# Kernel optimization log

Hardware: AMD Instinct MI355X
Metric: run time of the kernel (lower is better)

## Reference

```python
import jax, jax.numpy as jnp
import numpy as np

N_NODES = 50000
N_REL = 4
N_EDGE = 160000
H = 128
OUT = 100
L_HID = 2
N_QUERY = 8192


def setup_inputs() -> dict:
    key = jax.random.key(0)
    ks = jax.random.split(key, 10)
    s = 1.0 / np.sqrt(H)
    return {
        "feature": jax.random.normal(ks[0], (N_NODES, H), dtype=jnp.float32),
        "Wr_h": jax.random.normal(ks[1], (L_HID, N_REL, H, H), dtype=jnp.float32) * s,
        "Ws_h": jax.random.normal(ks[2], (L_HID, H, H), dtype=jnp.float32) * s,
        "Wr_o": jax.random.normal(ks[3], (N_REL, H, OUT), dtype=jnp.float32) * s,
        "Ws_o": jax.random.normal(ks[4], (H, OUT), dtype=jnp.float32) * s,
        "edge_src": jax.random.randint(ks[5], (N_REL, N_EDGE), 0, N_NODES, dtype=jnp.int64),
        "edge_dst": jax.random.randint(ks[6], (N_REL, N_EDGE), 0, N_NODES, dtype=jnp.int64),
        "head_idx": jax.random.randint(ks[7], (N_QUERY,), 0, N_NODES, dtype=jnp.int64),
        "tail_idx": jax.random.randint(ks[8], (N_QUERY,), 0, N_NODES, dtype=jnp.int64),
    }


def _rgcn_layer(h, edge_src, edge_dst, inv_deg, Wr, Ws, activate):
    # per-relation gather of source features: [R, E, H]
    msgs = h[edge_src]
    # per-relation scatter-add into destination nodes: [R, N, H]
    agg = jax.vmap(lambda m, d: jax.ops.segment_sum(m, d, num_segments=h.shape[0]))(msgs, edge_dst)
    agg = agg * inv_deg[..., None]  # mean (right) normalization per relation
    out = h @ Ws + jnp.einsum("rnh,rho->no", agg, Wr)
    return jax.nn.relu(out) if activate else out


def reference(feature, Wr_h, Ws_h, Wr_o, Ws_o, edge_src, edge_dst, head_idx, tail_idx):
    n = feature.shape[0]
    # per-relation in-degree, computed once (graph structure is fixed)
    deg = jax.vmap(lambda d: jax.ops.segment_sum(
        jnp.ones(d.shape, feature.dtype), d, num_segments=n))(edge_dst)  # [R, N]
    inv_deg = 1.0 / jnp.maximum(deg, 1.0)
    h = feature
    for l in range(Wr_h.shape[0]):
        h = _rgcn_layer(h, edge_src, edge_dst, inv_deg, Wr_h[l], Ws_h[l], activate=True)
    h = _rgcn_layer(h, edge_src, edge_dst, inv_deg, Wr_o, Ws_o, activate=False)
    heads = h[head_idx]  # [Q, OUT]
    tails = h[tail_idx]  # [Q, OUT]
    return (heads, tails)
```

## Files before the change

### kernel.cpp

```cpp
#include <hip/hip_runtime.h>
#include <hip/hip_bf16.h>

#define NN 50000
#define NR 4
#define NE 160000
#define HD 128
#define OD 100
#define NQ 8192
#define ELL_CAP 16
#define OVF_CAP 8192

#define NB_BUILD 2500
#define NB_CONV  6250
#define NB_PREPW 960

typedef __attribute__((ext_vector_type(8))) short bf16x8;
typedef __attribute__((ext_vector_type(4))) float f32x4;
typedef __attribute__((ext_vector_type(2))) float f32x2;
typedef __attribute__((ext_vector_type(4))) int int4v;

static __device__ __forceinline__ unsigned short f2bf(float f) {
    union { float f; unsigned int u; } v; v.f = f;
    unsigned int u = v.u;
    unsigned int r = u + 0x7FFFu + ((u >> 16) & 1u);
    return (unsigned short)(r >> 16);
}
static __device__ __forceinline__ float bflo(unsigned int v) {
    union { unsigned int u; float f; } x; x.u = v << 16; return x.f;
}
static __device__ __forceinline__ float bfhi(unsigned int v) {
    union { unsigned int u; float f; } x; x.u = v & 0xffff0000u; return x.f;
}


__global__ __launch_bounds__(256) void prep_merged_kernel(
        const int* __restrict__ edge_src, const int* __restrict__ edge_dst,
        int* __restrict__ deg, int* __restrict__ ell,
        int* __restrict__ ovf_cnt, int2* __restrict__ ovf,
        const float* __restrict__ feature, unsigned short* __restrict__ h,
        const float* __restrict__ Ws_h, const float* __restrict__ Wr_h,
        const float* __restrict__ Ws_o, const float* __restrict__ Wr_o,
        unsigned short* __restrict__ Wt) {
    const int b = blockIdx.x;
    if (b < NB_BUILD) {
        const int i = b * 256 + threadIdx.x;
        const int r = i / NE;
        const int key = (edge_dst[i] << 2) | r;
        const int src = edge_src[i];
        const int pos = atomicAdd(&deg[key], 1);
        if (pos < ELL_CAP) ell[key * ELL_CAP + pos] = src;
        else {
            const int op = atomicAdd(ovf_cnt, 1);
            if (op < OVF_CAP) ovf[op] = make_int2(key, src);
        }
    } else if (b < NB_BUILD + NB_CONV) {
        const int i = ((b - NB_BUILD) * 256 + threadIdx.x) * 4;
        h[i + 0] = f2bf(feature[i + 0]);
        h[i + 1] = f2bf(feature[i + 1]);
        h[i + 2] = f2bf(feature[i + 2]);
        h[i + 3] = f2bf(feature[i + 3]);
    } else {
        const int idx = (b - NB_BUILD - NB_CONV) * 256 + threadIdx.x;
        const int l = idx / (128 * 640);
        const int rem = idx % (128 * 640);
        const int c = rem / 640;
        const int k = rem % 640;
        float v = 0.0f;
        if (l < 2) {
            if (k < HD) v = Ws_h[(l * HD + k) * HD + c];
            else {
                int r = (k - HD) >> 7, kk = (k - HD) & 127;
                v = Wr_h[((l * NR + r) * HD + kk) * HD + c];
            }
        } else if (c < OD) {
            if (k < HD) v = Ws_o[k * OD + c];
            else {
                int r = (k - HD) >> 7, kk = (k - HD) & 127;
                v = Wr_o[(r * HD + kk) * OD + c];
            }
        }
        Wt[idx] = f2bf(v);
    }
}


template<int MODE>
__global__ __launch_bounds__(512, 8)
void fused_kernel(const unsigned short* __restrict__ h,
                  const unsigned short* __restrict__ Bt,
                  const int* __restrict__ deg,
                  const int* __restrict__ ell,
                  const int* __restrict__ ovf_cnt,
                  const int2* __restrict__ ovf,
                  void* __restrict__ outp, int M) {
    __shared__ __align__(16) char lds[40960];
    const int tid = threadIdx.x;
    const int m0 = blockIdx.x * 32;
    const int lane = tid & 63;
    const int w = tid >> 6;

    {
        const int row = tid >> 4, kb = (tid & 15) * 16;
        int gr = m0 + row; if (gr >= M) gr = M - 1;
        int4v v = *(const int4v*)((const char*)h + (size_t)gr * 256 + kb);
        *(int4v*)(lds + row * 256 + (kb ^ ((row & 7) << 4))) = v;
    }

    {
        const int g = lane >> 4, li = lane & 15;
        const char* hp = (const char*)h + li * 16;
        const int n0 = m0 + (w << 2);

#pragma unroll 1
        for (int i = 0; i < 4; ++i) {
            const int n = n0 + i;
            const int nc = (n < M) ? n : (M - 1);
            const int key = (nc << 2) | g;
            const int dg = (n < M) ? deg[key] : 0;
            const int e = (dg < ELL_CAP) ? dg : ELL_CAP;
            const int* eb = ell + ((size_t)key << 4);

            const int4v s03 = *(const int4v*)(eb);
            const int4v s47 = *(const int4v*)(eb + 4);

            int4v vj[8];
            const int4v z = {0, 0, 0, 0};
#pragma unroll
            for (int j = 0; j < 4; j++)
                vj[j] = (j < e) ? *(const int4v*)(hp + (size_t)s03[j] * 256) : z;
#pragma unroll
            for (int j = 0; j < 4; j++)
                vj[4 + j] = (4 + j < e) ? *(const int4v*)(hp + (size_t)s47[j] * 256) : z;
            __builtin_amdgcn_sched_barrier(0);

            f32x2 c0 = {0.f, 0.f}, c1 = {0.f, 0.f}, c2 = {0.f, 0.f}, c3 = {0.f, 0.f};
#pragma unroll
            for (int j = 0; j < 8; j++) {
                const unsigned int* vu = (const unsigned int*)&vj[j];
                c0 += (f32x2){bflo(vu[0]), bfhi(vu[0])};
                c1 += (f32x2){bflo(vu[1]), bfhi(vu[1])};
                c2 += (f32x2){bflo(vu[2]), bfhi(vu[2])};
                c3 += (f32x2){bflo(vu[3]), bfhi(vu[3])};
            }

            if (dg > 8) {
                const int4v s8  = *(const int4v*)(eb + 8);
                const int4v s12 = *(const int4v*)(eb + 12);
                int4v wj[8];
#pragma unroll
                for (int j = 0; j < 4; j++)
                    wj[j] = (8 + j < e) ? *(const int4v*)(hp + (size_t)s8[j] * 256) : z;
#pragma unroll
                for (int j = 0; j < 4; j++)
                    wj[4 + j] = (12 + j < e) ? *(const int4v*)(hp + (size_t)s12[j] * 256) : z;
#pragma unroll
                for (int j = 0; j < 8; j++) {
                    const unsigned int* vu = (const unsigned int*)&wj[j];
                    c0 += (f32x2){bflo(vu[0]), bfhi(vu[0])};
                    c1 += (f32x2){bflo(vu[1]), bfhi(vu[1])};
                    c2 += (f32x2){bflo(vu[2]), bfhi(vu[2])};
                    c3 += (f32x2){bflo(vu[3]), bfhi(vu[3])};
                }
            }

            if (dg > ELL_CAP) {
                int oc = ovf_cnt[0];
                if (oc > OVF_CAP) oc = OVF_CAP;
                for (int k = 0; k < oc; ++k) {
                    const int2 ov = ovf[k];
                    if (ov.x == key) {
                        const int4v v = *(const int4v*)(hp + (size_t)ov.y * 256);
                        const unsigned int* vu = (const unsigned int*)&v;
                        c0 += (f32x2){bflo(vu[0]), bfhi(vu[0])};
                        c1 += (f32x2){bflo(vu[1]), bfhi(vu[1])};
                        c2 += (f32x2){bflo(vu[2]), bfhi(vu[2])};
                        c3 += (f32x2){bflo(vu[3]), bfhi(vu[3])};
                    }
                }
            }

            const float inv = 1.0f / fmaxf((float)dg, 1.0f);
            unsigned int p0 = (unsigned int)f2bf(inv * c0[0]) | ((unsigned int)f2bf(inv * c0[1]) << 16);
            unsigned int p1 = (unsigned int)f2bf(inv * c1[0]) | ((unsigned int)f2bf(inv * c1[1]) << 16);
            unsigned int p2 = (unsigned int)f2bf(inv * c2[0]) | ((unsigned int)f2bf(inv * c2[1]) << 16);
            unsigned int p3 = (unsigned int)f2bf(inv * c3[0]) | ((unsigned int)f2bf(inv * c3[1]) << 16);
            const int row = (w << 2) + i;
            const int cb = g * 256 + li * 16;
            *(int4v*)(lds + 8192 + row * 1024 + (cb ^ ((row & 7) << 4))) =
                (int4v){(int)p0, (int)p1, (int)p2, (int)p3};
        }
    }

    const int lr = lane & 15;
    const int lg = lane >> 4;
    const char* bB = (const char*)Bt + (size_t)(w * 16 + lr) * 1280;
    bf16x8 bpre[4];
#pragma unroll
    for (int kb = 0; kb < 4; kb++)
        bpre[kb] = *(const bf16x8*)(bB + kb * 64 + lg * 16);

    __syncthreads();

    f32x4 acc[2];
    acc[0] = (f32x4){0.f, 0.f, 0.f, 0.f};
    acc[1] = (f32x4){0.f, 0.f, 0.f, 0.f};

    __builtin_amdgcn_s_setprio(1);
#pragma unroll
    for (int kb = 0; kb < 20; ++kb) {
        const int kByte = kb * 64 + lg * 16;
        bf16x8 bfr = (kb < 4) ? bpre[kb] : *(const bf16x8*)(bB + kByte);
#pragma unroll
        for (int mi = 0; mi < 2; mi++) {
            const int row = mi * 16 + lr;
            int off;
            if (kb < 4) off = row * 256 + (kByte ^ ((row & 7) << 4));
            else        off = 8192 + row * 1024 + ((kByte - 256) ^ ((row & 7) << 4));
            bf16x8 af = *(const bf16x8*)(lds + off);
            acc[mi] = __builtin_amdgcn_mfma_f32_16x16x32_bf16(af, bfr, acc[mi], 0, 0, 0);
        }
    }
    __builtin_amdgcn_s_setprio(0);

    __syncthreads();

    if (MODE == 0) {
#pragma unroll
        for (int mi = 0; mi < 2; mi++) {
            const int col = w * 16 + lr;
#pragma unroll
            for (int j = 0; j < 4; j++) {
                const int row = mi * 16 + lg * 4 + j;
                *(unsigned short*)(lds + row * 256 + ((col * 2) ^ ((row & 7) << 4))) =
                    f2bf(fmaxf(acc[mi][j], 0.f));
            }
        }
        __syncthreads();
        unsigned short* o = (unsigned short*)outp;
        const int row = tid >> 4, kb = (tid & 15) * 16;
        const int grow = m0 + row;
        if (grow < M)
            *(int4v*)((char*)o + (size_t)grow * 256 + kb) =
                *(const int4v*)(lds + row * 256 + (kb ^ ((row & 7) << 4)));
    } else {
#pragma unroll
        for (int mi = 0; mi < 2; mi++) {
            const int col = w * 16 + lr;
#pragma unroll
            for (int j = 0; j < 4; j++) {
                const int row = mi * 16 + lg * 4 + j;
                *(float*)(lds + row * 512 + ((col * 4) ^ ((row & 7) << 4))) = acc[mi][j];
            }
        }
        __syncthreads();
        float* o = (float*)outp;
#pragma unroll
        for (int i = 0; i < 2; i++) {
            const int c = tid + i * 512;
            const int row = c >> 5, o16 = (c & 31) * 16;
            const int grow = m0 + row;
            if (grow < M)
                *(int4v*)((char*)o + (size_t)grow * 512 + o16) =
                    *(const int4v*)(lds + row * 512 + (o16 ^ ((row & 7) << 4)));
        }
    }
}


__global__ __launch_bounds__(256) void gather_out_kernel(const float* __restrict__ hOut,
                                                         const int* __restrict__ head,
                                                         const int* __restrict__ tail,
                                                         float* __restrict__ out) {
    const int gid = blockIdx.x * 256 + threadIdx.x;
    const int q = gid >> 5, c = gid & 31;
    if (q >= 2 * NQ || c >= 25) return;
    const int node = (q < NQ) ? head[q] : tail[q - NQ];
    f32x4 v = *(const f32x4*)(hOut + (size_t)node * 128 + c * 4);
    *(f32x4*)(out + (size_t)q * OD + c * 4) = v;
}


extern "C" void kernel_launch(void* const* d_in, const int* in_sizes, int n_in,
                              void* d_out, int out_size, void* d_ws, size_t ws_size,
                              hipStream_t stream) {
    const float* feature = (const float*)d_in[0];
    const float* Wr_h    = (const float*)d_in[1];
    const float* Ws_h    = (const float*)d_in[2];
    const float* Wr_o    = (const float*)d_in[3];
    const float* Ws_o    = (const float*)d_in[4];
    const int* edge_src  = (const int*)d_in[5];
    const int* edge_dst  = (const int*)d_in[6];
    const int* head_idx  = (const int*)d_in[7];
    const int* tail_idx  = (const int*)d_in[8];
    float* out = (float*)d_out;

    char* ws = (char*)d_ws;
    size_t off = 0;
    auto alloc = [&](size_t bytes) -> void* {
        void* p = ws + off;
        off += (bytes + 255) & ~(size_t)255;
        return p;
    };
    unsigned short* hA   = (unsigned short*)alloc((size_t)NN * HD * 2);
    unsigned short* hB   = (unsigned short*)alloc((size_t)NN * HD * 2);
    float*          hOut = (float*)alloc((size_t)NN * 128 * 4);
    unsigned short* Wt   = (unsigned short*)alloc((size_t)3 * 128 * 640 * 2);
    int*            deg  = (int*)alloc((size_t)NR * NN * 4);
    int*            ovfc = (int*)alloc(256);
    int*            ell  = (int*)alloc((size_t)NR * NN * ELL_CAP * 4);
    int2*           ovf  = (int2*)alloc((size_t)OVF_CAP * 8);
    (void)ws_size;

    hipMemsetAsync(deg, 0, (size_t)NR * NN * 4 + 256, stream);
    prep_merged_kernel<<<NB_BUILD + NB_CONV + NB_PREPW, 256, 0, stream>>>(
        edge_src, edge_dst, deg, ell, ovfc, ovf,
        feature, hA, Ws_h, Wr_h, Ws_o, Wr_o, Wt);

    const int fblocks = (NN + 31) / 32;
    unsigned short* WtH0 = Wt;
    unsigned short* WtH1 = Wt + 128 * 640;
    unsigned short* WtO  = Wt + 2 * 128 * 640;

    fused_kernel<0><<<fblocks, 512, 0, stream>>>(hA, WtH0, deg, ell, ovfc, ovf, hB, NN);
    fused_kernel<0><<<fblocks, 512, 0, stream>>>(hB, WtH1, deg, ell, ovfc, ovf, hA, NN);
    fused_kernel<1><<<fblocks, 512, 0, stream>>>(hA, WtO,  deg, ell, ovfc, ovf, hOut, NN);

    gather_out_kernel<<<(2 * NQ * 32 + 255) / 256, 256, 0, stream>>>(hOut, head_idx, tail_idx, out);
}
```

Baseline: 220.6 us.

## Split ELL into lo/hi halves and double block threads to 1024

The ELL adjacency table is split into two arrays of 8 slots each, so the common low-degree path reads a compact 32-byte row and only touches the high half when degree exceeds 8. The fused aggregate+GEMM kernel moves to 1024 threads per block. Each wave now aggregates 2 nodes instead of 4, with both nodes' degree and index loads hoisted ahead of the loop, and computes one 16x16 MFMA tile instead of two. The sched_barrier is removed. The aim is more memory-level parallelism in the irregular gather and less serial work per wave. The cost is a tighter register budget per thread under launch_bounds(1024,2) and more waves competing for the same LDS tile.

```diff
diff --git a/kernel.cpp b/kernel.cpp
--- a/kernel.cpp
+++ b/kernel.cpp
@@ -35,7 +35,7 @@
 
 __global__ __launch_bounds__(256) void prep_merged_kernel(
         const int* __restrict__ edge_src, const int* __restrict__ edge_dst,
-        int* __restrict__ deg, int* __restrict__ ell,
+        int* __restrict__ deg, int* __restrict__ ell_lo, int* __restrict__ ell_hi,
         int* __restrict__ ovf_cnt, int2* __restrict__ ovf,
         const float* __restrict__ feature, unsigned short* __restrict__ h,
         const float* __restrict__ Ws_h, const float* __restrict__ Wr_h,
@@ -48,7 +48,8 @@
         const int key = (edge_dst[i] << 2) | r;
         const int src = edge_src[i];
         const int pos = atomicAdd(&deg[key], 1);
-        if (pos < ELL_CAP) ell[key * ELL_CAP + pos] = src;
+        if (pos < 8)             ell_lo[key * 8 + pos] = src;
+        else if (pos < ELL_CAP)  ell_hi[key * 8 + (pos - 8)] = src;
         else {
             const int op = atomicAdd(ovf_cnt, 1);
             if (op < OVF_CAP) ovf[op] = make_int2(key, src);
@@ -85,11 +86,12 @@
 
 
 template<int MODE>
-__global__ __launch_bounds__(512, 8)
+__global__ __launch_bounds__(1024, 2)
 void fused_kernel(const unsigned short* __restrict__ h,
                   const unsigned short* __restrict__ Bt,
                   const int* __restrict__ deg,
-                  const int* __restrict__ ell,
+                  const int* __restrict__ ell_lo,
+                  const int* __restrict__ ell_hi,
                   const int* __restrict__ ovf_cnt,
                   const int2* __restrict__ ovf,
                   void* __restrict__ outp, int M) {
@@ -99,7 +101,7 @@
     const int lane = tid & 63;
     const int w = tid >> 6;
 
-    {
+    if (tid < 512) {
         const int row = tid >> 4, kb = (tid & 15) * 16;
         int gr = m0 + row; if (gr >= M) gr = M - 1;
         int4v v = *(const int4v*)((const char*)h + (size_t)gr * 256 + kb);
@@ -109,29 +111,33 @@
     {
         const int g = lane >> 4, li = lane & 15;
         const char* hp = (const char*)h + li * 16;
-        const int n0 = m0 + (w << 2);
-
-#pragma unroll 1
-        for (int i = 0; i < 4; ++i) {
-            const int n = n0 + i;
-            const int nc = (n < M) ? n : (M - 1);
-            const int key = (nc << 2) | g;
-            const int dg = (n < M) ? deg[key] : 0;
-            const int e = (dg < ELL_CAP) ? dg : ELL_CAP;
-            const int* eb = ell + ((size_t)key << 4);
-
-            const int4v s03 = *(const int4v*)(eb);
-            const int4v s47 = *(const int4v*)(eb + 4);
+        const int n0 = m0 + (w << 1);
+
+        const int nA = n0, nB = n0 + 1;
+        const int kA = (((nA < M) ? nA : (M - 1)) << 2) | g;
+        const int kB = (((nB < M) ? nB : (M - 1)) << 2) | g;
+        const int dgA = (nA < M) ? deg[kA] : 0;
+        const int dgB = (nB < M) ? deg[kB] : 0;
+        const int4v sA0 = *(const int4v*)(ell_lo + ((size_t)kA << 3));
+        const int4v sA1 = *(const int4v*)(ell_lo + ((size_t)kA << 3) + 4);
+        const int4v sB0 = *(const int4v*)(ell_lo + ((size_t)kB << 3));
+        const int4v sB1 = *(const int4v*)(ell_lo + ((size_t)kB << 3) + 4);
+        const int4v z = {0, 0, 0, 0};
+
+#pragma unroll
+        for (int i = 0; i < 2; ++i) {
+            const int dg  = i ? dgB : dgA;
+            const int key = i ? kB : kA;
+            const int4v s03 = i ? sB0 : sA0;
+            const int4v s47 = i ? sB1 : sA1;
 
             int4v vj[8];
-            const int4v z = {0, 0, 0, 0};
 #pragma unroll
             for (int j = 0; j < 4; j++)
-                vj[j] = (j < e) ? *(const int4v*)(hp + (size_t)s03[j] * 256) : z;
+                vj[j] = (j < dg) ? *(const int4v*)(hp + (size_t)s03[j] * 256) : z;
 #pragma unroll
             for (int j = 0; j < 4; j++)
-                vj[4 + j] = (4 + j < e) ? *(const int4v*)(hp + (size_t)s47[j] * 256) : z;
-            __builtin_amdgcn_sched_barrier(0);
+                vj[4 + j] = (4 + j < dg) ? *(const int4v*)(hp + (size_t)s47[j] * 256) : z;
 
             f32x2 c0 = {0.f, 0.f}, c1 = {0.f, 0.f}, c2 = {0.f, 0.f}, c3 = {0.f, 0.f};
 #pragma unroll
@@ -144,15 +150,16 @@
             }
 
             if (dg > 8) {
-                const int4v s8  = *(const int4v*)(eb + 8);
-                const int4v s12 = *(const int4v*)(eb + 12);
+                const int e = (dg < ELL_CAP) ? dg : ELL_CAP;
+                const int4v h8  = *(const int4v*)(ell_hi + ((size_t)key << 3));
+                const int4v h12 = *(const int4v*)(ell_hi + ((size_t)key << 3) + 4);
                 int4v wj[8];
 #pragma unroll
                 for (int j = 0; j < 4; j++)
-                    wj[j] = (8 + j < e) ? *(const int4v*)(hp + (size_t)s8[j] * 256) : z;
+                    wj[j] = (8 + j < e) ? *(const int4v*)(hp + (size_t)h8[j] * 256) : z;
 #pragma unroll
                 for (int j = 0; j < 4; j++)
-                    wj[4 + j] = (12 + j < e) ? *(const int4v*)(hp + (size_t)s12[j] * 256) : z;
+                    wj[4 + j] = (12 + j < e) ? *(const int4v*)(hp + (size_t)h12[j] * 256) : z;
 #pragma unroll
                 for (int j = 0; j < 8; j++) {
                     const unsigned int* vu = (const unsigned int*)&wj[j];
@@ -184,7 +191,7 @@
             unsigned int p1 = (unsigned int)f2bf(inv * c1[0]) | ((unsigned int)f2bf(inv * c1[1]) << 16);
             unsigned int p2 = (unsigned int)f2bf(inv * c2[0]) | ((unsigned int)f2bf(inv * c2[1]) << 16);
             unsigned int p3 = (unsigned int)f2bf(inv * c3[0]) | ((unsigned int)f2bf(inv * c3[1]) << 16);
-            const int row = (w << 2) + i;
+            const int row = (w << 1) + i;
             const int cb = g * 256 + li * 16;
             *(int4v*)(lds + 8192 + row * 1024 + (cb ^ ((row & 7) << 4))) =
                 (int4v){(int)p0, (int)p1, (int)p2, (int)p3};
@@ -193,7 +200,9 @@
 
     const int lr = lane & 15;
     const int lg = lane >> 4;
-    const char* bB = (const char*)Bt + (size_t)(w * 16 + lr) * 1280;
+    const int rh = w >> 3;
+    const int cg = w & 7;
+    const char* bB = (const char*)Bt + (size_t)(cg * 16 + lr) * 1280;
     bf16x8 bpre[4];
 #pragma unroll
     for (int kb = 0; kb < 4; kb++)
@@ -201,68 +210,55 @@
 
     __syncthreads();
 
-    f32x4 acc[2];
-    acc[0] = (f32x4){0.f, 0.f, 0.f, 0.f};
-    acc[1] = (f32x4){0.f, 0.f, 0.f, 0.f};
+    f32x4 acc = {0.f, 0.f, 0.f, 0.f};
+    const int arow = rh * 16 + lr;
 
     __builtin_amdgcn_s_setprio(1);
 #pragma unroll
     for (int kb = 0; kb < 20; ++kb) {
         const int kByte = kb * 64 + lg * 16;
         bf16x8 bfr = (kb < 4) ? bpre[kb] : *(const bf16x8*)(bB + kByte);
-#pragma unroll
-        for (int mi = 0; mi < 2; mi++) {
-            const int row = mi * 16 + lr;
-            int off;
-            if (kb < 4) off = row * 256 + (kByte ^ ((row & 7) << 4));
-            else        off = 8192 + row * 1024 + ((kByte - 256) ^ ((row & 7) << 4));
-            bf16x8 af = *(const bf16x8*)(lds + off);
-            acc[mi] = __builtin_amdgcn_mfma_f32_16x16x32_bf16(af, bfr, acc[mi], 0, 0, 0);
-        }
+        int off;
+        if (kb < 4) off = arow * 256 + (kByte ^ ((arow & 7) << 4));
+        else        off = 8192 + arow * 1024 + ((kByte - 256) ^ ((arow & 7) << 4));
+        bf16x8 af = *(const bf16x8*)(lds + off);
+        acc = __builtin_amdgcn_mfma_f32_16x16x32_bf16(af, bfr, acc, 0, 0, 0);
     }
     __builtin_amdgcn_s_setprio(0);
 
     __syncthreads();
 
     if (MODE == 0) {
-#pragma unroll
-        for (int mi = 0; mi < 2; mi++) {
-            const int col = w * 16 + lr;
-#pragma unroll
-            for (int j = 0; j < 4; j++) {
-                const int row = mi * 16 + lg * 4 + j;
-                *(unsigned short*)(lds + row * 256 + ((col * 2) ^ ((row & 7) << 4))) =
-                    f2bf(fmaxf(acc[mi][j], 0.f));
-            }
+        const int col = cg * 16 + lr;
+#pragma unroll
+        for (int j = 0; j < 4; j++) {
+            const int row = rh * 16 + lg * 4 + j;
+            *(unsigned short*)(lds + row * 256 + ((col * 2) ^ ((row & 7) << 4))) =
+                f2bf(fmaxf(acc[j], 0.f));
         }
         __syncthreads();
-        unsigned short* o = (unsigned short*)outp;
-        const int row = tid >> 4, kb = (tid & 15) * 16;
+        if (tid < 512) {
+            unsigned short* o = (unsigned short*)outp;
+            const int row = tid >> 4, kb = (tid & 15) * 16;
+            const int grow = m0 + row;
+            if (grow < M)
+                *(int4v*)((char*)o + (size_t)grow * 256 + kb) =
+                    *(const int4v*)(lds + row * 256 + (kb ^ ((row & 7) << 4)));
+        }
+    } else {
+        const int col = cg * 16 + lr;
+#pragma unroll
+        for (int j = 0; j < 4; j++) {
+            const int row = rh * 16 + lg * 4 + j;
+            *(float*)(lds + row * 512 + ((col * 4) ^ ((row & 7) << 4))) = acc[j];
+        }
+        __syncthreads();
+        float* o = (float*)outp;
+        const int row = tid >> 5, o16 = (tid & 31) * 16;
         const int grow = m0 + row;
         if (grow < M)
-            *(int4v*)((char*)o + (size_t)grow * 256 + kb) =
-                *(const int4v*)(lds + row * 256 + (kb ^ ((row & 7) << 4)));
-    } else {
-#pragma unroll
-        for (int mi = 0; mi < 2; mi++) {
-            const int col = w * 16 + lr;
-#pragma unroll
-            for (int j = 0; j < 4; j++) {
-                const int row = mi * 16 + lg * 4 + j;
-                *(float*)(lds + row * 512 + ((col * 4) ^ ((row & 7) << 4))) = acc[mi][j];
-            }
-        }
-        __syncthreads();
-        float* o = (float*)outp;
-#pragma unroll
-        for (int i = 0; i < 2; i++) {
-            const int c = tid + i * 512;
-            const int row = c >> 5, o16 = (c & 31) * 16;
-            const int grow = m0 + row;
-            if (grow < M)
-                *(int4v*)((char*)o + (size_t)grow * 512 + o16) =
-                    *(const int4v*)(lds + row * 512 + (o16 ^ ((row & 7) << 4)));
-        }
+            *(int4v*)((char*)o + (size_t)grow * 512 + o16) =
+                *(const int4v*)(lds + row * 512 + (o16 ^ ((row & 7) << 4)));
     }
 }
 
@@ -307,13 +303,14 @@
     unsigned short* Wt   = (unsigned short*)alloc((size_t)3 * 128 * 640 * 2);
     int*            deg  = (int*)alloc((size_t)NR * NN * 4);
     int*            ovfc = (int*)alloc(256);
-    int*            ell  = (int*)alloc((size_t)NR * NN * ELL_CAP * 4);
+    int*            elLo = (int*)alloc((size_t)NR * NN * 8 * 4);
+    int*            elHi = (int*)alloc((size_t)NR * NN * 8 * 4);
     int2*           ovf  = (int2*)alloc((size_t)OVF_CAP * 8);
     (void)ws_size;
 
     hipMemsetAsync(deg, 0, (size_t)NR * NN * 4 + 256, stream);
     prep_merged_kernel<<<NB_BUILD + NB_CONV + NB_PREPW, 256, 0, stream>>>(
-        edge_src, edge_dst, deg, ell, ovfc, ovf,
+        edge_src, edge_dst, deg, elLo, elHi, ovfc, ovf,
         feature, hA, Ws_h, Wr_h, Ws_o, Wr_o, Wt);
 
     const int fblocks = (NN + 31) / 32;
@@ -321,9 +318,9 @@
     unsigned short* WtH1 = Wt + 128 * 640;
     unsigned short* WtO  = Wt + 2 * 128 * 640;
 
-    fused_kernel<0><<<fblocks, 512, 0, stream>>>(hA, WtH0, deg, ell, ovfc, ovf, hB, NN);
-    fused_kernel<0><<<fblocks, 512, 0, stream>>>(hB, WtH1, deg, ell, ovfc, ovf, hA, NN);
-    fused_kernel<1><<<fblocks, 512, 0, stream>>>(hA, WtO,  deg, ell, ovfc, ovf, hOut, NN);
+    fused_kernel<0><<<fblocks, 1024, 0, stream>>>(hA, WtH0, deg, elLo, elHi, ovfc, ovf, hB, NN);
+    fused_kernel<0><<<fblocks, 1024, 0, stream>>>(hB, WtH1, deg, elLo, elHi, ovfc, ovf, hA, NN);
+    fused_kernel<1><<<fblocks, 1024, 0, stream>>>(hA, WtO,  deg, elLo, elHi, ovfc, ovf, hOut, NN);
 
     gather_out_kernel<<<(2 * NQ * 32 + 255) / 256, 256, 0, stream>>>(hOut, head_idx, tail_idx, out);
 }
```

New measurement: 324.5 us. 1.47x slower.

## Split ELL into lo/hi halves and prefetch next node's neighbor indices

Applied to the files above, without the earlier changes.

Splits the 16-slot ELL adjacency into two arrays of 8 slots each, so the common first-8 index loads touch a dense 32-byte row per key and the rarely used upper half sits elsewhere. The aggregation loop now loads all degrees first, then prefetches the next node's low-half neighbor indices while gathering the current node's features. This software pipeline hides the index-load latency that sat in front of the dependent feature gathers. It adds register pressure from the unrolled loop and the carried index vectors.

```diff
diff --git a/kernel.cpp b/kernel.cpp
--- a/kernel.cpp
+++ b/kernel.cpp
@@ -35,7 +35,7 @@
 
 __global__ __launch_bounds__(256) void prep_merged_kernel(
         const int* __restrict__ edge_src, const int* __restrict__ edge_dst,
-        int* __restrict__ deg, int* __restrict__ ell,
+        int* __restrict__ deg, int* __restrict__ ell_lo, int* __restrict__ ell_hi,
         int* __restrict__ ovf_cnt, int2* __restrict__ ovf,
         const float* __restrict__ feature, unsigned short* __restrict__ h,
         const float* __restrict__ Ws_h, const float* __restrict__ Wr_h,
@@ -48,7 +48,8 @@
         const int key = (edge_dst[i] << 2) | r;
         const int src = edge_src[i];
         const int pos = atomicAdd(&deg[key], 1);
-        if (pos < ELL_CAP) ell[key * ELL_CAP + pos] = src;
+        if (pos < 8)             ell_lo[key * 8 + pos] = src;
+        else if (pos < ELL_CAP)  ell_hi[key * 8 + (pos - 8)] = src;
         else {
             const int op = atomicAdd(ovf_cnt, 1);
             if (op < OVF_CAP) ovf[op] = make_int2(key, src);
@@ -89,7 +90,8 @@
 void fused_kernel(const unsigned short* __restrict__ h,
                   const unsigned short* __restrict__ Bt,
                   const int* __restrict__ deg,
-                  const int* __restrict__ ell,
+                  const int* __restrict__ ell_lo,
+                  const int* __restrict__ ell_hi,
                   const int* __restrict__ ovf_cnt,
                   const int2* __restrict__ ovf,
                   void* __restrict__ outp, int M) {
@@ -111,26 +113,36 @@
         const char* hp = (const char*)h + li * 16;
         const int n0 = m0 + (w << 2);
 
-#pragma unroll 1
-        for (int i = 0; i < 4; ++i) {
+        int ks[4], dgs[4];
+#pragma unroll
+        for (int i = 0; i < 4; i++) {
             const int n = n0 + i;
             const int nc = (n < M) ? n : (M - 1);
-            const int key = (nc << 2) | g;
-            const int dg = (n < M) ? deg[key] : 0;
-            const int e = (dg < ELL_CAP) ? dg : ELL_CAP;
-            const int* eb = ell + ((size_t)key << 4);
-
-            const int4v s03 = *(const int4v*)(eb);
-            const int4v s47 = *(const int4v*)(eb + 4);
+            ks[i] = (nc << 2) | g;
+            dgs[i] = (n < M) ? deg[ks[i]] : 0;
+        }
+
+        const int4v z = {0, 0, 0, 0};
+        int4v sc0 = *(const int4v*)(ell_lo + ((size_t)ks[0] << 3));
+        int4v sc1 = *(const int4v*)(ell_lo + ((size_t)ks[0] << 3) + 4);
+
+#pragma unroll
+        for (int i = 0; i < 4; ++i) {
+            int4v sn0 = z, sn1 = z;
+            if (i < 3) {
+                sn0 = *(const int4v*)(ell_lo + ((size_t)ks[i + 1] << 3));
+                sn1 = *(const int4v*)(ell_lo + ((size_t)ks[i + 1] << 3) + 4);
+            }
+            const int dg  = dgs[i];
+            const int key = ks[i];
 
             int4v vj[8];
-            const int4v z = {0, 0, 0, 0};
 #pragma unroll
             for (int j = 0; j < 4; j++)
-                vj[j] = (j < e) ? *(const int4v*)(hp + (size_t)s03[j] * 256) : z;
+                vj[j] = (j < dg) ? *(const int4v*)(hp + (size_t)sc0[j] * 256) : z;
 #pragma unroll
             for (int j = 0; j < 4; j++)
-                vj[4 + j] = (4 + j < e) ? *(const int4v*)(hp + (size_t)s47[j] * 256) : z;
+                vj[4 + j] = (4 + j < dg) ? *(const int4v*)(hp + (size_t)sc1[j] * 256) : z;
             __builtin_amdgcn_sched_barrier(0);
 
             f32x2 c0 = {0.f, 0.f}, c1 = {0.f, 0.f}, c2 = {0.f, 0.f}, c3 = {0.f, 0.f};
@@ -144,15 +156,16 @@
             }
 
             if (dg > 8) {
-                const int4v s8  = *(const int4v*)(eb + 8);
-                const int4v s12 = *(const int4v*)(eb + 12);
+                const int e = (dg < ELL_CAP) ? dg : ELL_CAP;
+                const int4v h8  = *(const int4v*)(ell_hi + ((size_t)key << 3));
+                const int4v h12 = *(const int4v*)(ell_hi + ((size_t)key << 3) + 4);
                 int4v wj[8];
 #pragma unroll
                 for (int j = 0; j < 4; j++)
-                    wj[j] = (8 + j < e) ? *(const int4v*)(hp + (size_t)s8[j] * 256) : z;
+                    wj[j] = (8 + j < e) ? *(const int4v*)(hp + (size_t)h8[j] * 256) : z;
 #pragma unroll
                 for (int j = 0; j < 4; j++)
-                    wj[4 + j] = (12 + j < e) ? *(const int4v*)(hp + (size_t)s12[j] * 256) : z;
+                    wj[4 + j] = (12 + j < e) ? *(const int4v*)(hp + (size_t)h12[j] * 256) : z;
 #pragma unroll
                 for (int j = 0; j < 8; j++) {
                     const unsigned int* vu = (const unsigned int*)&wj[j];
@@ -188,6 +201,8 @@
             const int cb = g * 256 + li * 16;
             *(int4v*)(lds + 8192 + row * 1024 + (cb ^ ((row & 7) << 4))) =
                 (int4v){(int)p0, (int)p1, (int)p2, (int)p3};
+
+            sc0 = sn0; sc1 = sn1;
         }
     }
 
@@ -307,13 +322,14 @@
     unsigned short* Wt   = (unsigned short*)alloc((size_t)3 * 128 * 640 * 2);
     int*            deg  = (int*)alloc((size_t)NR * NN * 4);
     int*            ovfc = (int*)alloc(256);
-    int*            ell  = (int*)alloc((size_t)NR * NN * ELL_CAP * 4);
+    int*            elLo = (int*)alloc((size_t)NR * NN * 8 * 4);
+    int*            elHi = (int*)alloc((size_t)NR * NN * 8 * 4);
     int2*           ovf  = (int2*)alloc((size_t)OVF_CAP * 8);
     (void)ws_size;
 
     hipMemsetAsync(deg, 0, (size_t)NR * NN * 4 + 256, stream);
     prep_merged_kernel<<<NB_BUILD + NB_CONV + NB_PREPW, 256, 0, stream>>>(
-        edge_src, edge_dst, deg, ell, ovfc, ovf,
+        edge_src, edge_dst, deg, elLo, elHi, ovfc, ovf,
         feature, hA, Ws_h, Wr_h, Ws_o, Wr_o, Wt);
 
     const int fblocks = (NN + 31) / 32;
@@ -321,9 +337,9 @@
     unsigned short* WtH1 = Wt + 128 * 640;
     unsigned short* WtO  = Wt + 2 * 128 * 640;
 
-    fused_kernel<0><<<fblocks, 512, 0, stream>>>(hA, WtH0, deg, ell, ovfc, ovf, hB, NN);
-    fused_kernel<0><<<fblocks, 512, 0, stream>>>(hB, WtH1, deg, ell, ovfc, ovf, hA, NN);
-    fused_kernel<1><<<fblocks, 512, 0, stream>>>(hA, WtO,  deg, ell, ovfc, ovf, hOut, NN);
+    fused_kernel<0><<<fblocks, 512, 0, stream>>>(hA, WtH0, deg, elLo, elHi, ovfc, ovf, hB, NN);
+    fused_kernel<0><<<fblocks, 512, 0, stream>>>(hB, WtH1, deg, elLo, elHi, ovfc, ovf, hA, NN);
+    fused_kernel<1><<<fblocks, 512, 0, stream>>>(hA, WtO,  deg, elLo, elHi, ovfc, ovf, hOut, NN);
 
     gather_out_kernel<<<(2 * NQ * 32 + 255) / 256, 256, 0, stream>>>(hOut, head_idx, tail_idx, out);
 }
```

After: 248.7 us. 1.13x slower.
